# Performance work log

Measured on AMD Instinct MI355X. Metric: run time of the kernel, lower is better.

## Reference

```python
import jax, jax.numpy as jnp
import numpy as np

N = 100000
F_IN = 128
HID = 128
E = 1600000


def gcn_conv(x, W, b, src, dst, dinv):
    # PyG GCNConv: h = x @ W; out_i = sum_j norm_ij * h_j (incl. self-loop) + b
    h = x @ W  # [N, H]
    norm = dinv[src] * dinv[dst]  # [E]
    msg = h[src] * norm[:, None]  # [E, H]
    agg = jax.ops.segment_sum(msg, dst, num_segments=N)
    agg = agg + h * (dinv * dinv)[:, None]  # self-loop contribution
    return agg + b


def setup_inputs() -> dict:
    key = jax.random.key(0)
    k1, k2, k3, k4, k5 = jax.random.split(key, 5)
    x = jax.random.normal(k1, (N, F_IN), dtype=jnp.float32)
    edge_index = jax.random.randint(k2, (2, E), 0, N, dtype=jnp.int64)
    s = 1.0 / np.sqrt(F_IN)
    W1 = jax.random.normal(k3, (F_IN, HID), dtype=jnp.float32) * s
    b1 = jnp.zeros((HID,), dtype=jnp.float32)
    sh = 1.0 / np.sqrt(HID)
    W2 = jax.random.normal(k4, (HID, HID), dtype=jnp.float32) * sh
    b2 = jnp.zeros((HID,), dtype=jnp.float32)
    Wfc = jax.random.normal(k5, (HID, 2), dtype=jnp.float32) * sh
    bfc = jnp.zeros((2,), dtype=jnp.float32)
    return {"x": x, "edge_index": edge_index, "W1": W1, "b1": b1,
            "W2": W2, "b2": b2, "Wfc": Wfc, "bfc": bfc}


def reference(x, edge_index, W1, b1, W2, b2, Wfc, bfc):
    src, dst = edge_index[0], edge_index[1]
    # degree with self-loops (edge weight 1), computed on target nodes
    deg = jax.ops.segment_sum(jnp.ones((E,), jnp.float32), dst, num_segments=N) + 1.0
    dinv = jax.lax.rsqrt(deg)
    h = jax.nn.relu(gcn_conv(x, W1, b1, src, dst, dinv))
    h = jax.nn.relu(gcn_conv(h, W2, b2, src, dst, dinv))
    logits = h @ Wfc + bfc  # [N, 2]
    return jax.nn.log_softmax(logits, axis=1)
```

## Files before the change

### kernel.cpp

```cpp
#include <hip/hip_runtime.h>
#include <math.h>

#define N_NODES 100000
#define FDIM 128
#define E_EDGES 1600000
#define NSCAN_BLKS ((N_NODES + 1023) / 1024)
#define NPASS 8
#define PASS_NODES 12500

typedef unsigned short bf16_t;
typedef __attribute__((ext_vector_type(8))) short short8;
typedef __attribute__((ext_vector_type(4))) float f32x4;

__device__ inline bf16_t f2bf(float f) {
    unsigned int u = __float_as_uint(f);
    return (bf16_t)((u + 0x7fffu + ((u >> 16) & 1u)) >> 16);
}
__device__ inline float2 bfpair(unsigned int u) {
    return make_float2(__uint_as_float(u << 16), __uint_as_float(u & 0xffff0000u));
}

__global__ __launch_bounds__(256) void hist_kernel(const int* __restrict__ dst,
                                                   int* __restrict__ cnt) {
    int pass = blockIdx.x & (NPASS - 1);
    int e = (blockIdx.x >> 3) * 256 + threadIdx.x;
    if (e >= E_EDGES) return;
    int d = dst[e];
    if ((unsigned)(d - pass * PASS_NODES) < (unsigned)PASS_NODES)
        atomicAdd(&cnt[d], 1);
}

__global__ __launch_bounds__(256) void scan1(const int* __restrict__ cnt,
                                             int* __restrict__ excl,
                                             int* __restrict__ bsum) {
    __shared__ int lds[256];
    const int b = blockIdx.x, t = threadIdx.x;
    const int base = b * 1024 + t * 4;
    int v[4];
#pragma unroll
    for (int q = 0; q < 4; ++q) {
        int i = base + q;
        v[q] = (i < N_NODES) ? cnt[i] : 0;
    }
    int tsum = v[0] + v[1] + v[2] + v[3];
    lds[t] = tsum;
    __syncthreads();
    for (int off = 1; off < 256; off <<= 1) {
        int x = lds[t];
        int y = (t >= off) ? lds[t - off] : 0;
        __syncthreads();
        lds[t] = x + y;
        __syncthreads();
    }
    int texcl = lds[t] - tsum;
    if (t == 255) bsum[b] = lds[t];
    int run = texcl;
#pragma unroll
    for (int q = 0; q < 4; ++q) {
        int i = base + q;
        if (i < N_NODES) excl[i] = run;
        run += v[q];
    }
}

__global__ __launch_bounds__(128) void scan2(int* __restrict__ bsum) {
    __shared__ int lds[128];
    const int t = threadIdx.x;
    int v = (t < NSCAN_BLKS) ? bsum[t] : 0;
    lds[t] = v;
    __syncthreads();
    for (int off = 1; off < 128; off <<= 1) {
        int x = lds[t];
        int y = (t >= off) ? lds[t - off] : 0;
        __syncthreads();
        lds[t] = x + y;
        __syncthreads();
    }
    if (t < NSCAN_BLKS) bsum[t] = lds[t] - v;
}

__global__ __launch_bounds__(256) void scan3(int* __restrict__ rowptr,
                                             const int* __restrict__ bsum,
                                             const int* __restrict__ cnt,
                                             float* __restrict__ dinv) {
    int i = blockIdx.x * blockDim.x + threadIdx.x;
    if (i < N_NODES) {
        rowptr[i] += bsum[i >> 10];
        dinv[i] = rsqrtf((float)cnt[i] + 1.0f);
    }
    if (i == 0) rowptr[N_NODES] = E_EDGES;
}

__global__ __launch_bounds__(256) void scatter_kernel(const int* __restrict__ src,
                                                      const int* __restrict__ dst,
                                                      const int* __restrict__ rowptr,
                                                      const float* __restrict__ dinv,
                                                      int* __restrict__ cursor,
                                                      int2* __restrict__ emeta) {
    int pass = blockIdx.x & (NPASS - 1);
    int e = (blockIdx.x >> 3) * 256 + threadIdx.x;
    if (e >= E_EDGES) return;
    int d = dst[e];
    if ((unsigned)(d - pass * PASS_NODES) < (unsigned)PASS_NODES) {
        int s = src[e];
        int p = rowptr[d] + atomicAdd(&cursor[d], 1);
        float nrm = dinv[s] * dinv[d];
        emeta[p] = make_int2(s, __float_as_int(nrm));
    }
}

__global__ __launch_bounds__(256) void wcvt_kernel(const float* __restrict__ W,
                                                   bf16_t* __restrict__ Wt) {
    int idx = blockIdx.x * 256 + threadIdx.x;
    int k = idx >> 7, c = idx & 127;
    Wt[c * 128 + k] = f2bf(W[idx]);
}

template <bool A_IS_F32>
__global__ __launch_bounds__(256) void gemm_mfma(const void* __restrict__ Aptr,
                                                 const bf16_t* __restrict__ Wt,
                                                 bf16_t* __restrict__ H) {
    const int tid = threadIdx.x;
    const int wave = tid >> 6;
    const int l = tid & 63;
    const int r = l & 15;
    const int g = l >> 4;
    const int row0 = (blockIdx.x * 4 + wave) * 16;
    const int arow = min(row0 + r, N_NODES - 1);

    f32x4 acc[8];
#pragma unroll
    for (int ct = 0; ct < 8; ++ct) acc[ct] = (f32x4){0.f, 0.f, 0.f, 0.f};

#pragma unroll
    for (int ks = 0; ks < 4; ++ks) {
        const int kbase = ks * 32 + g * 8;
        short8 a;
        if constexpr (A_IS_F32) {
            const float* X = (const float*)Aptr;
            const float4 x0 = *((const float4*)(X + (size_t)arow * 128 + kbase));
            const float4 x1 = *((const float4*)(X + (size_t)arow * 128 + kbase + 4));
            a[0] = (short)f2bf(x0.x); a[1] = (short)f2bf(x0.y);
            a[2] = (short)f2bf(x0.z); a[3] = (short)f2bf(x0.w);
            a[4] = (short)f2bf(x1.x); a[5] = (short)f2bf(x1.y);
            a[6] = (short)f2bf(x1.z); a[7] = (short)f2bf(x1.w);
        } else {
            const bf16_t* X = (const bf16_t*)Aptr;
            a = *((const short8*)(X + (size_t)arow * 128 + kbase));
        }
#pragma unroll
        for (int ct = 0; ct < 8; ++ct) {
            short8 b = *((const short8*)(Wt + (ct * 16 + r) * 128 + kbase));
            acc[ct] = __builtin_amdgcn_mfma_f32_16x16x32_bf16(a, b, acc[ct], 0, 0, 0);
        }
    }

#pragma unroll
    for (int j = 0; j < 4; ++j) {
        const int row = row0 + g * 4 + j;
        if (row < N_NODES) {
            bf16_t* hp = H + (size_t)row * 128 + r;
#pragma unroll
            for (int ct = 0; ct < 8; ++ct) hp[ct * 16] = f2bf(acc[ct][j]);
        }
    }
}

__global__ __launch_bounds__(256) void agg_kernel(const int* __restrict__ rowptr,
                                                  const int2* __restrict__ emeta,
                                                  const float* __restrict__ dinv,
                                                  const bf16_t* __restrict__ h,
                                                  const float* __restrict__ bias,
                                                  bf16_t* __restrict__ out) {
    int gid = blockIdx.x * blockDim.x + threadIdx.x;
    int node = gid >> 6;
    int lane = gid & 63;
    if (node >= N_NODES) return;
    float dd = dinv[node];
    float2 v = bfpair(((const unsigned*)(h + (size_t)node * 128))[lane]);
    float sc = dd * dd;
    float accx = v.x * sc, accy = v.y * sc;
    int j = rowptr[node];
    const int end = rowptr[node + 1];
    for (; j + 3 < end; j += 4) {
        int2 m0 = emeta[j], m1 = emeta[j + 1], m2 = emeta[j + 2], m3 = emeta[j + 3];
        float n0 = __int_as_float(m0.y), n1 = __int_as_float(m1.y);
        float n2 = __int_as_float(m2.y), n3 = __int_as_float(m3.y);
        float2 v0 = bfpair(((const unsigned*)(h + (size_t)m0.x * 128))[lane]);
        float2 v1 = bfpair(((const unsigned*)(h + (size_t)m1.x * 128))[lane]);
        float2 v2 = bfpair(((const unsigned*)(h + (size_t)m2.x * 128))[lane]);
        float2 v3 = bfpair(((const unsigned*)(h + (size_t)m3.x * 128))[lane]);
        accx += v0.x * n0 + v1.x * n1 + v2.x * n2 + v3.x * n3;
        accy += v0.y * n0 + v1.y * n1 + v2.y * n2 + v3.y * n3;
    }
    for (; j < end; ++j) {
        int2 m0 = emeta[j];
        float n0 = __int_as_float(m0.y);
        float2 v0 = bfpair(((const unsigned*)(h + (size_t)m0.x * 128))[lane]);
        accx += v0.x * n0;
        accy += v0.y * n0;
    }
    float2 b = ((const float2*)bias)[lane];
    accx = fmaxf(accx + b.x, 0.f);
    accy = fmaxf(accy + b.y, 0.f);
    unsigned o = (unsigned)f2bf(accx) | ((unsigned)f2bf(accy) << 16);
    ((unsigned*)(out + (size_t)node * 128))[lane] = o;
}

__global__ __launch_bounds__(256) void agg_fc_kernel(const int* __restrict__ rowptr,
                                                     const int2* __restrict__ emeta,
                                                     const float* __restrict__ dinv,
                                                     const bf16_t* __restrict__ h,
                                                     const float* __restrict__ bias,
                                                     const float* __restrict__ Wfc,
                                                     const float* __restrict__ bfc,
                                                     float* __restrict__ out) {
    int gid = blockIdx.x * blockDim.x + threadIdx.x;
    int node = gid >> 6;
    int lane = gid & 63;
    if (node >= N_NODES) return;
    float dd = dinv[node];
    float2 v = bfpair(((const unsigned*)(h + (size_t)node * 128))[lane]);
    float sc = dd * dd;
    float accx = v.x * sc, accy = v.y * sc;
    int j = rowptr[node];
    const int end = rowptr[node + 1];
    for (; j + 3 < end; j += 4) {
        int2 m0 = emeta[j], m1 = emeta[j + 1], m2 = emeta[j + 2], m3 = emeta[j + 3];
        float n0 = __int_as_float(m0.y), n1 = __int_as_float(m1.y);
        float n2 = __int_as_float(m2.y), n3 = __int_as_float(m3.y);
        float2 v0 = bfpair(((const unsigned*)(h + (size_t)m0.x * 128))[lane]);
        float2 v1 = bfpair(((const unsigned*)(h + (size_t)m1.x * 128))[lane]);
        float2 v2 = bfpair(((const unsigned*)(h + (size_t)m2.x * 128))[lane]);
        float2 v3 = bfpair(((const unsigned*)(h + (size_t)m3.x * 128))[lane]);
        accx += v0.x * n0 + v1.x * n1 + v2.x * n2 + v3.x * n3;
        accy += v0.y * n0 + v1.y * n1 + v2.y * n2 + v3.y * n3;
    }
    for (; j < end; ++j) {
        int2 m0 = emeta[j];
        float n0 = __int_as_float(m0.y);
        float2 v0 = bfpair(((const unsigned*)(h + (size_t)m0.x * 128))[lane]);
        accx += v0.x * n0;
        accy += v0.y * n0;
    }
    float2 b = ((const float2*)bias)[lane];
    accx = fmaxf(accx + b.x, 0.f);
    accy = fmaxf(accy + b.y, 0.f);
    int k0 = lane * 2;
    float a0 = accx * Wfc[k0 * 2 + 0] + accy * Wfc[(k0 + 1) * 2 + 0];
    float a1 = accx * Wfc[k0 * 2 + 1] + accy * Wfc[(k0 + 1) * 2 + 1];
#pragma unroll
    for (int off = 32; off > 0; off >>= 1) {
        a0 += __shfl_down(a0, off);
        a1 += __shfl_down(a1, off);
    }
    if (lane == 0) {
        float l0 = a0 + bfc[0];
        float l1 = a1 + bfc[1];
        float m = fmaxf(l0, l1);
        float lse = m + logf(expf(l0 - m) + expf(l1 - m));
        out[(size_t)node * 2 + 0] = l0 - lse;
        out[(size_t)node * 2 + 1] = l1 - lse;
    }
}

extern "C" void kernel_launch(void* const* d_in, const int* in_sizes, int n_in,
                              void* d_out, int out_size, void* d_ws, size_t ws_size,
                              hipStream_t stream) {
    const float* x   = (const float*)d_in[0];
    const int*   ei  = (const int*)d_in[1];
    const float* W1  = (const float*)d_in[2];
    const float* b1  = (const float*)d_in[3];
    const float* W2  = (const float*)d_in[4];
    const float* b2  = (const float*)d_in[5];
    const float* Wfc = (const float*)d_in[6];
    const float* bfc = (const float*)d_in[7];
    float* out = (float*)d_out;

    const int* src = ei;
    const int* dst = ei + E_EDGES;

    char* wp = (char*)d_ws;
    auto carve = [&](size_t bytes) -> char* {
        char* p = wp;
        wp += (bytes + 255) & ~(size_t)255;
        return p;
    };
    int*    cnt    = (int*)carve(N_NODES * 4);
    int*    rowptr = (int*)carve((N_NODES + 1) * 4);
    int*    cursor = (int*)carve(N_NODES * 4);
    int*    bsum   = (int*)carve(128 * 4);
    int2*   emeta  = (int2*)carve((size_t)E_EDGES * 8);
    float*  dinv   = (float*)carve(N_NODES * 4);
    bf16_t* hbuf   = (bf16_t*)carve((size_t)N_NODES * FDIM * 2);
    bf16_t* x2buf  = (bf16_t*)carve((size_t)N_NODES * FDIM * 2);
    bf16_t* Wt1    = (bf16_t*)carve(128 * 128 * 2);
    bf16_t* Wt2    = (bf16_t*)carve(128 * 128 * 2);

    const int NN_BLK = (N_NODES + 255) / 256;
    const int NODE_WAVE_BLK = (N_NODES * 64 + 255) / 256;
    const int EDGE_PASS_BLK = ((E_EDGES + 255) / 256) * NPASS;
    const int GEMM_BLK = (N_NODES + 63) / 64;

    hipMemsetAsync(cnt, 0, N_NODES * sizeof(int), stream);
    hipMemsetAsync(cursor, 0, N_NODES * sizeof(int), stream);
    hist_kernel<<<EDGE_PASS_BLK, 256, 0, stream>>>(dst, cnt);
    scan1<<<NSCAN_BLKS, 256, 0, stream>>>(cnt, rowptr, bsum);
    scan2<<<1, 128, 0, stream>>>(bsum);
    scan3<<<NN_BLK, 256, 0, stream>>>(rowptr, bsum, cnt, dinv);
    scatter_kernel<<<EDGE_PASS_BLK, 256, 0, stream>>>(src, dst, rowptr, dinv,
                                                      cursor, emeta);

    wcvt_kernel<<<64, 256, 0, stream>>>(W1, Wt1);
    wcvt_kernel<<<64, 256, 0, stream>>>(W2, Wt2);

    gemm_mfma<true><<<GEMM_BLK, 256, 0, stream>>>(x, Wt1, hbuf);
    agg_kernel<<<NODE_WAVE_BLK, 256, 0, stream>>>(rowptr, emeta, dinv, hbuf, b1, x2buf);

    gemm_mfma<false><<<GEMM_BLK, 256, 0, stream>>>(x2buf, Wt2, hbuf);
    agg_fc_kernel<<<NODE_WAVE_BLK, 256, 0, stream>>>(rowptr, emeta, dinv, hbuf, b2,
                                                     Wfc, bfc, out);
}
```

Baseline: 470.2 us.

## Split aggregation across feature halves with prefetched edge metadata, separate FC kernel

Aggregation now runs one wave per node per 64-feature half: each lane gathers a single bf16 (a 2-byte load) instead of a packed pair, and the grid is doubled. The kernel is unrolled by 8 and software-prefetches the next group of edge metadata to keep more gathers in flight. The fused aggregation plus FC is split so the second layer writes an intermediate buffer that a separate FC/log-softmax kernel then reads. In exchange, edge metadata is read twice per node, gather loads are narrower, there is an extra 25 MB intermediate write and read, and one more kernel launch.

```diff
diff --git a/kernel.cpp b/kernel.cpp
--- a/kernel.cpp
+++ b/kernel.cpp
@@ -15,6 +15,9 @@
 __device__ inline bf16_t f2bf(float f) {
     unsigned int u = __float_as_uint(f);
     return (bf16_t)((u + 0x7fffu + ((u >> 16) & 1u)) >> 16);
+}
+__device__ inline float bf2f(bf16_t u) {
+    return __uint_as_float(((unsigned)u) << 16);
 }
 __device__ inline float2 bfpair(unsigned int u) {
     return make_float2(__uint_as_float(u << 16), __uint_as_float(u & 0xffff0000u));
@@ -166,89 +169,82 @@
     }
 }
 
-__global__ __launch_bounds__(256) void agg_kernel(const int* __restrict__ rowptr,
-                                                  const int2* __restrict__ emeta,
-                                                  const float* __restrict__ dinv,
-                                                  const bf16_t* __restrict__ h,
-                                                  const float* __restrict__ bias,
-                                                  bf16_t* __restrict__ out) {
+__global__ __launch_bounds__(256) void agg_half_kernel(const int* __restrict__ rowptr,
+                                                       const int2* __restrict__ emeta,
+                                                       const float* __restrict__ dinv,
+                                                       const bf16_t* __restrict__ h,
+                                                       const float* __restrict__ bias,
+                                                       bf16_t* __restrict__ out) {
+    const int b = blockIdx.x;
+    const int wave = threadIdx.x >> 6;
+    const int lane = threadIdx.x & 63;
+    const int half = (b >> 2) & 1;
+    const int idx  = (b >> 3) * 4 + (b & 3);
+    const int node = idx * 4 + wave;
+    if (node >= N_NODES) return;
+    const int f = half * 64 + lane;
+    const bf16_t* __restrict__ hc = h + f;
+
+    float dd = dinv[node];
+    float acc = dd * dd * bf2f(hc[(size_t)node * 128]);
+
+    int j = rowptr[node];
+    const int end = rowptr[node + 1];
+
+    int2 m0, m1, m2, m3, m4, m5, m6, m7;
+    bool have = (j + 8 <= end);
+    if (have) {
+        m0 = emeta[j + 0]; m1 = emeta[j + 1]; m2 = emeta[j + 2]; m3 = emeta[j + 3];
+        m4 = emeta[j + 4]; m5 = emeta[j + 5]; m6 = emeta[j + 6]; m7 = emeta[j + 7];
+    }
+    while (have) {
+        const int jn = j + 8;
+        const bool nxt = (jn + 8 <= end);
+        int2 t0, t1, t2, t3, t4, t5, t6, t7;
+        if (nxt) {
+            t0 = emeta[jn + 0]; t1 = emeta[jn + 1]; t2 = emeta[jn + 2]; t3 = emeta[jn + 3];
+            t4 = emeta[jn + 4]; t5 = emeta[jn + 5]; t6 = emeta[jn + 6]; t7 = emeta[jn + 7];
+        }
+        float v0 = bf2f(hc[(size_t)m0.x * 128]);
+        float v1 = bf2f(hc[(size_t)m1.x * 128]);
+        float v2 = bf2f(hc[(size_t)m2.x * 128]);
+        float v3 = bf2f(hc[(size_t)m3.x * 128]);
+        float v4 = bf2f(hc[(size_t)m4.x * 128]);
+        float v5 = bf2f(hc[(size_t)m5.x * 128]);
+        float v6 = bf2f(hc[(size_t)m6.x * 128]);
+        float v7 = bf2f(hc[(size_t)m7.x * 128]);
+        acc += v0 * __int_as_float(m0.y) + v1 * __int_as_float(m1.y)
+             + v2 * __int_as_float(m2.y) + v3 * __int_as_float(m3.y)
+             + v4 * __int_as_float(m4.y) + v5 * __int_as_float(m5.y)
+             + v6 * __int_as_float(m6.y) + v7 * __int_as_float(m7.y);
+        j = jn;
+        have = nxt;
+        if (nxt) {
+            m0 = t0; m1 = t1; m2 = t2; m3 = t3;
+            m4 = t4; m5 = t5; m6 = t6; m7 = t7;
+        }
+    }
+    for (; j < end; ++j) {
+        int2 m = emeta[j];
+        acc += bf2f(hc[(size_t)m.x * 128]) * __int_as_float(m.y);
+    }
+
+    acc = fmaxf(acc + bias[f], 0.f);
+    out[(size_t)node * 128 + f] = f2bf(acc);
+}
+
+__global__ __launch_bounds__(256) void fc_kernel(const bf16_t* __restrict__ x,
+                                                 const float* __restrict__ Wfc,
+                                                 const float* __restrict__ bfc,
+                                                 float* __restrict__ out) {
     int gid = blockIdx.x * blockDim.x + threadIdx.x;
     int node = gid >> 6;
     int lane = gid & 63;
     if (node >= N_NODES) return;
-    float dd = dinv[node];
-    float2 v = bfpair(((const unsigned*)(h + (size_t)node * 128))[lane]);
-    float sc = dd * dd;
-    float accx = v.x * sc, accy = v.y * sc;
-    int j = rowptr[node];
-    const int end = rowptr[node + 1];
-    for (; j + 3 < end; j += 4) {
-        int2 m0 = emeta[j], m1 = emeta[j + 1], m2 = emeta[j + 2], m3 = emeta[j + 3];
-        float n0 = __int_as_float(m0.y), n1 = __int_as_float(m1.y);
-        float n2 = __int_as_float(m2.y), n3 = __int_as_float(m3.y);
-        float2 v0 = bfpair(((const unsigned*)(h + (size_t)m0.x * 128))[lane]);
-        float2 v1 = bfpair(((const unsigned*)(h + (size_t)m1.x * 128))[lane]);
-        float2 v2 = bfpair(((const unsigned*)(h + (size_t)m2.x * 128))[lane]);
-        float2 v3 = bfpair(((const unsigned*)(h + (size_t)m3.x * 128))[lane]);
-        accx += v0.x * n0 + v1.x * n1 + v2.x * n2 + v3.x * n3;
-        accy += v0.y * n0 + v1.y * n1 + v2.y * n2 + v3.y * n3;
-    }
-    for (; j < end; ++j) {
-        int2 m0 = emeta[j];
-        float n0 = __int_as_float(m0.y);
-        float2 v0 = bfpair(((const unsigned*)(h + (size_t)m0.x * 128))[lane]);
-        accx += v0.x * n0;
-        accy += v0.y * n0;
-    }
-    float2 b = ((const float2*)bias)[lane];
-    accx = fmaxf(accx + b.x, 0.f);
-    accy = fmaxf(accy + b.y, 0.f);
-    unsigned o = (unsigned)f2bf(accx) | ((unsigned)f2bf(accy) << 16);
-    ((unsigned*)(out + (size_t)node * 128))[lane] = o;
-}
-
-__global__ __launch_bounds__(256) void agg_fc_kernel(const int* __restrict__ rowptr,
-                                                     const int2* __restrict__ emeta,
-                                                     const float* __restrict__ dinv,
-                                                     const bf16_t* __restrict__ h,
-                                                     const float* __restrict__ bias,
-                                                     const float* __restrict__ Wfc,
-                                                     const float* __restrict__ bfc,
-                                                     float* __restrict__ out) {
-    int gid = blockIdx.x * blockDim.x + threadIdx.x;
-    int node = gid >> 6;
-    int lane = gid & 63;
-    if (node >= N_NODES) return;
-    float dd = dinv[node];
-    float2 v = bfpair(((const unsigned*)(h + (size_t)node * 128))[lane]);
-    float sc = dd * dd;
-    float accx = v.x * sc, accy = v.y * sc;
-    int j = rowptr[node];
-    const int end = rowptr[node + 1];
-    for (; j + 3 < end; j += 4) {
-        int2 m0 = emeta[j], m1 = emeta[j + 1], m2 = emeta[j + 2], m3 = emeta[j + 3];
-        float n0 = __int_as_float(m0.y), n1 = __int_as_float(m1.y);
-        float n2 = __int_as_float(m2.y), n3 = __int_as_float(m3.y);
-        float2 v0 = bfpair(((const unsigned*)(h + (size_t)m0.x * 128))[lane]);
-        float2 v1 = bfpair(((const unsigned*)(h + (size_t)m1.x * 128))[lane]);
-        float2 v2 = bfpair(((const unsigned*)(h + (size_t)m2.x * 128))[lane]);
-        float2 v3 = bfpair(((const unsigned*)(h + (size_t)m3.x * 128))[lane]);
-        accx += v0.x * n0 + v1.x * n1 + v2.x * n2 + v3.x * n3;
-        accy += v0.y * n0 + v1.y * n1 + v2.y * n2 + v3.y * n3;
-    }
-    for (; j < end; ++j) {
-        int2 m0 = emeta[j];
-        float n0 = __int_as_float(m0.y);
-        float2 v0 = bfpair(((const unsigned*)(h + (size_t)m0.x * 128))[lane]);
-        accx += v0.x * n0;
-        accy += v0.y * n0;
-    }
-    float2 b = ((const float2*)bias)[lane];
-    accx = fmaxf(accx + b.x, 0.f);
-    accy = fmaxf(accy + b.y, 0.f);
+    float2 v = bfpair(((const unsigned*)(x + (size_t)node * 128))[lane]);
     int k0 = lane * 2;
-    float a0 = accx * Wfc[k0 * 2 + 0] + accy * Wfc[(k0 + 1) * 2 + 0];
-    float a1 = accx * Wfc[k0 * 2 + 1] + accy * Wfc[(k0 + 1) * 2 + 1];
+    float a0 = v.x * Wfc[k0 * 2 + 0] + v.y * Wfc[(k0 + 1) * 2 + 0];
+    float a1 = v.x * Wfc[k0 * 2 + 1] + v.y * Wfc[(k0 + 1) * 2 + 1];
 #pragma unroll
     for (int off = 32; off > 0; off >>= 1) {
         a0 += __shfl_down(a0, off);
@@ -294,6 +290,7 @@
     float*  dinv   = (float*)carve(N_NODES * 4);
     bf16_t* hbuf   = (bf16_t*)carve((size_t)N_NODES * FDIM * 2);
     bf16_t* x2buf  = (bf16_t*)carve((size_t)N_NODES * FDIM * 2);
+    bf16_t* x3buf  = (bf16_t*)carve((size_t)N_NODES * FDIM * 2);
     bf16_t* Wt1    = (bf16_t*)carve(128 * 128 * 2);
     bf16_t* Wt2    = (bf16_t*)carve(128 * 128 * 2);
 
@@ -301,6 +298,7 @@
     const int NODE_WAVE_BLK = (N_NODES * 64 + 255) / 256;
     const int EDGE_PASS_BLK = ((E_EDGES + 255) / 256) * NPASS;
     const int GEMM_BLK = (N_NODES + 63) / 64;
+    const int AGG_BLK = 50000;
 
     hipMemsetAsync(cnt, 0, N_NODES * sizeof(int), stream);
     hipMemsetAsync(cursor, 0, N_NODES * sizeof(int), stream);
@@ -315,9 +313,10 @@
     wcvt_kernel<<<64, 256, 0, stream>>>(W2, Wt2);
 
     gemm_mfma<true><<<GEMM_BLK, 256, 0, stream>>>(x, Wt1, hbuf);
-    agg_kernel<<<NODE_WAVE_BLK, 256, 0, stream>>>(rowptr, emeta, dinv, hbuf, b1, x2buf);
+    agg_half_kernel<<<AGG_BLK, 256, 0, stream>>>(rowptr, emeta, dinv, hbuf, b1, x2buf);
 
     gemm_mfma<false><<<GEMM_BLK, 256, 0, stream>>>(x2buf, Wt2, hbuf);
-    agg_fc_kernel<<<NODE_WAVE_BLK, 256, 0, stream>>>(rowptr, emeta, dinv, hbuf, b2,
-                                                     Wfc, bfc, out);
-}
+    agg_half_kernel<<<AGG_BLK, 256, 0, stream>>>(rowptr, emeta, dinv, hbuf, b2, x3buf);
+
+    fc_kernel<<<NODE_WAVE_BLK, 256, 0, stream>>>(x3buf, Wfc, bfc, out);
+}
```

After: 627.4 us. 33.4% more time.
